# Performance work log

Measured on AMD Instinct MI355X. Metric: run time of the kernel, lower is better.

## Reference

```python
import jax
jax.config.update("jax_enable_x64", True)
import jax.numpy as jnp
import numpy as np

B = 1_000_000

def _generators():
    # 8 sl(3) basis elements, each scaled by its (unit) weight, float64.
    e = np.zeros((8, 3, 3), dtype=np.float64)
    e[0, 0, 2] = 1.0                      # x translation
    e[1, 1, 2] = 1.0                      # y translation
    e[2, 0, 1] = -1.0; e[2, 1, 0] = 1.0   # rotation
    e[3, 0, 0] = 1.0; e[3, 1, 1] = 1.0; e[3, 2, 2] = -2.0  # scale
    e[4, 0, 0] = 1.0; e[4, 1, 1] = -1.0   # stretch
    e[5, 0, 1] = 1.0; e[5, 1, 0] = 1.0    # shear
    e[6, 2, 0] = 1.0                      # x keystone
    e[7, 2, 1] = 1.0                      # y keystone
    weights = np.ones((8,), dtype=np.float64)  # all weight kwargs default to 1.0
    return jnp.asarray(e * weights[:, None, None])

_GEN = _generators()

def setup_inputs() -> dict:
    key = jax.random.key(0)
    lie_vectors = jax.random.normal(key, (B, 8), dtype=jnp.float32)
    return {"lie_vectors": lie_vectors}

def reference(lie_vectors) -> jnp.ndarray:
    # Weighted sum of generators in float64: (B,8) x (8,3,3) -> (B,3,3)
    A = jnp.einsum("bk,kij->bij", lie_vectors.astype(jnp.float64), _GEN)
    # Batched matrix exponential of tiny 3x3 matrices
    H = jax.vmap(jax.scipy.linalg.expm)(A)
    # Homogeneous normalization by the (2,2) entry
    H = H / H[:, 2:3, 2:3]
    return H.astype(jnp.float32)
```

## Files before the change

kernel.cpp:

```cpp
#include <hip/hip_runtime.h>
#include <math.h>

__device__ __forceinline__ void mm3(const double* __restrict__ A,
                                    const double* __restrict__ Bm,
                                    double* __restrict__ C) {
#pragma unroll
    for (int i = 0; i < 3; ++i) {
#pragma unroll
        for (int j = 0; j < 3; ++j) {
            C[i*3+j] = fma(A[i*3+0], Bm[0*3+j],
                       fma(A[i*3+1], Bm[1*3+j],
                           A[i*3+2] * Bm[2*3+j]));
        }
    }
}

#define BLOCK 256

__global__ __launch_bounds__(BLOCK) void lie_expm_kernel(const float* __restrict__ v,
                                                         float* __restrict__ out,
                                                         int n) {
    __shared__ float lds[BLOCK * 9];

    int tid = threadIdx.x;
    int gid = blockIdx.x * BLOCK + tid;
    bool active = gid < n;

    float oloc[9];

    if (active) {
        const float4* vv = reinterpret_cast<const float4*>(v);
        float4 p0 = vv[2*(size_t)gid + 0];
        float4 p1 = vv[2*(size_t)gid + 1];
        double x0 = p0.x, x1 = p0.y, x2 = p0.z, x3 = p0.w;
        double x4 = p1.x, x5 = p1.y, x6 = p1.z, x7 = p1.w;

        double A[9];
        A[0] = x3 + x4;  A[1] = x5 - x2;  A[2] = x0;
        A[3] = x2 + x5;  A[4] = x3 - x4;  A[5] = x1;
        A[6] = x6;       A[7] = x7;       A[8] = -2.0 * x3;

        double c0 = fabs(A[0]) + fabs(A[3]) + fabs(A[6]);
        double c1 = fabs(A[1]) + fabs(A[4]) + fabs(A[7]);
        double c2 = fabs(A[2]) + fabs(A[5]) + fabs(A[8]);
        double nrm = fmax(c0, fmax(c1, c2));

        const double theta13 = 5.371920351148152;
        double r = nrm * (1.0 / theta13);
        int s = 0;
        if (r > 1.0) {
            int hi = __double2hiint(r);
            s = ((hi >> 20) & 0x7ff) - 1023 + 1;
        }
        double sc = __hiloint2double((1023 - s) << 20, 0);
#pragma unroll
        for (int i = 0; i < 9; ++i) A[i] *= sc;

        const double b0  = 64764752532480000.0, b1  = 32382376266240000.0;
        const double b2  = 7771770303897600.0,  b3  = 1187353796428800.0;
        const double b4  = 129060195264000.0,   b5  = 10559470521600.0;
        const double b6  = 670442572800.0,      b7  = 33522128640.0;
        const double b8  = 1323241920.0,        b9  = 40840800.0;
        const double b10 = 960960.0,            b11 = 16380.0;
        const double b12 = 182.0,               b13 = 1.0;

        double A2[9], A4[9], A6[9];
        mm3(A, A, A2);
        mm3(A2, A2, A4);
        mm3(A4, A2, A6);

        double W[9], V[9];
#pragma unroll
        for (int i = 0; i < 9; ++i)
            W[i] = fma(b12, A6[i], fma(b10, A4[i], b8 * A2[i]));
        mm3(A6, W, V);
#pragma unroll
        for (int i = 0; i < 9; ++i)
            V[i] += fma(b6, A6[i], fma(b4, A4[i], b2 * A2[i]));
        V[0] += b0; V[4] += b0; V[8] += b0;

        double Z[9], U[9];
#pragma unroll
        for (int i = 0; i < 9; ++i)
            W[i] = fma(b13, A6[i], fma(b11, A4[i], b9 * A2[i]));
        mm3(A6, W, Z);
#pragma unroll
        for (int i = 0; i < 9; ++i)
            Z[i] += fma(b7, A6[i], fma(b5, A4[i], b3 * A2[i]));
        Z[0] += b1; Z[4] += b1; Z[8] += b1;
        mm3(A, Z, U);

        double M[9], R[9];
#pragma unroll
        for (int i = 0; i < 9; ++i) { M[i] = V[i] - U[i]; R[i] = V[i] + U[i]; }

        double inv[9];
        inv[0] = fma(M[4], M[8], -M[5]*M[7]);
        inv[1] = fma(M[2], M[7], -M[1]*M[8]);
        inv[2] = fma(M[1], M[5], -M[2]*M[4]);
        inv[3] = fma(M[5], M[6], -M[3]*M[8]);
        inv[4] = fma(M[0], M[8], -M[2]*M[6]);
        inv[5] = fma(M[2], M[3], -M[0]*M[5]);
        inv[6] = fma(M[3], M[7], -M[4]*M[6]);
        inv[7] = fma(M[1], M[6], -M[0]*M[7]);
        inv[8] = fma(M[0], M[4], -M[1]*M[3]);
        double det = fma(M[0], inv[0], fma(M[1], inv[3], M[2]*inv[6]));
        double rd = 1.0 / det;
#pragma unroll
        for (int i = 0; i < 9; ++i) inv[i] *= rd;

        double E[9], T[9];
        mm3(inv, R, E);

        for (int i = 0; i < s; ++i) {
            mm3(E, E, T);
#pragma unroll
            for (int j = 0; j < 9; ++j) E[j] = T[j];
        }

        double invh = 1.0 / E[8];
#pragma unroll
        for (int i = 0; i < 9; ++i) oloc[i] = (float)(E[i] * invh);
    }

    if (active) {
#pragma unroll
        for (int j = 0; j < 9; ++j) lds[tid * 9 + j] = oloc[j];
    }
    __syncthreads();

    size_t base = (size_t)blockIdx.x * (BLOCK * 9);
    int count = n - blockIdx.x * BLOCK;
    if (count > BLOCK) count = BLOCK;
    int total = count * 9;
#pragma unroll
    for (int i = 0; i < 9; ++i) {
        int idx = i * BLOCK + tid;
        if (idx < total) out[base + idx] = lds[idx];
    }
}

extern "C" void kernel_launch(void* const* d_in, const int* in_sizes, int n_in,
                              void* d_out, int out_size, void* d_ws, size_t ws_size,
                              hipStream_t stream) {
    const float* v = (const float*)d_in[0];
    float* out = (float*)d_out;
    int n = in_sizes[0] / 8;
    int grid = (n + BLOCK - 1) / BLOCK;
    lie_expm_kernel<<<grid, BLOCK, 0, stream>>>(v, out, n);
}
```

Measured before the change: 88.49 us.

## Evaluate Padé expm in the Cayley-Hamilton polynomial basis of traceless A

Because A is traceless (sl(3)), every matrix polynomial in A reduces to e0*I + e1*A + e2*A^2 with p = tr(A^2)/2 and q = det(A). The Padé numerator and denominator, the solve, and the repeated squaring are all done on these three coefficients, using Horner steps, a small structured 3x3 cofactor solve and coefficient squaring, rather than full 3x3 double matrix products. The full matrix is rebuilt only once at the end. This cuts FP64 arithmetic and register pressure a lot. The trade-off is possible precision differences, and the determinant scaling is skipped when s < 3, since it cancels in the final normalization.

```diff
diff --git a/kernel.cpp b/kernel.cpp
--- a/kernel.cpp
+++ b/kernel.cpp
@@ -1,21 +1,15 @@
 #include <hip/hip_runtime.h>
 #include <math.h>
 
-__device__ __forceinline__ void mm3(const double* __restrict__ A,
-                                    const double* __restrict__ Bm,
-                                    double* __restrict__ C) {
-#pragma unroll
-    for (int i = 0; i < 3; ++i) {
-#pragma unroll
-        for (int j = 0; j < 3; ++j) {
-            C[i*3+j] = fma(A[i*3+0], Bm[0*3+j],
-                       fma(A[i*3+1], Bm[1*3+j],
-                           A[i*3+2] * Bm[2*3+j]));
-        }
+#define BLOCK 256
+
+#define QSTEP(a0, a1, a2, bn)                         \
+    {                                                 \
+        double n0 = fma(q, a1, bn);                   \
+        double n1 = fma(p, a1, q * (a2));             \
+        double n2 = fma(p, a2, a0);                   \
+        a0 = n0; a1 = n1; a2 = n2;                    \
     }
-}
-
-#define BLOCK 256
 
 __global__ __launch_bounds__(BLOCK) void lie_expm_kernel(const float* __restrict__ v,
                                                          float* __restrict__ out,
@@ -30,8 +24,8 @@
 
     if (active) {
         const float4* vv = reinterpret_cast<const float4*>(v);
-        float4 p0 = vv[2*(size_t)gid + 0];
-        float4 p1 = vv[2*(size_t)gid + 1];
+        float4 p0 = vv[2 * (size_t)gid + 0];
+        float4 p1 = vv[2 * (size_t)gid + 1];
         double x0 = p0.x, x1 = p0.y, x2 = p0.z, x3 = p0.w;
         double x4 = p1.x, x5 = p1.y, x6 = p1.z, x7 = p1.w;
 
@@ -56,6 +50,22 @@
 #pragma unroll
         for (int i = 0; i < 9; ++i) A[i] *= sc;
 
+        double A2[9];
+#pragma unroll
+        for (int i = 0; i < 3; ++i) {
+#pragma unroll
+            for (int j = 0; j < 3; ++j) {
+                A2[i * 3 + j] = fma(A[i * 3 + 0], A[0 * 3 + j],
+                                fma(A[i * 3 + 1], A[1 * 3 + j],
+                                    A[i * 3 + 2] * A[2 * 3 + j]));
+            }
+        }
+
+        double p = 0.5 * (A2[0] + A2[4] + A2[8]);
+        double q = fma(A[0], fma(A[4], A[8], -A[5] * A[7]),
+                   fma(-A[1], fma(A[3], A[8], -A[5] * A[6]),
+                       A[2] * fma(A[3], A[7], -A[4] * A[6])));
+
         const double b0  = 64764752532480000.0, b1  = 32382376266240000.0;
         const double b2  = 7771770303897600.0,  b3  = 1187353796428800.0;
         const double b4  = 129060195264000.0,   b5  = 10559470521600.0;
@@ -64,63 +74,72 @@
         const double b10 = 960960.0,            b11 = 16380.0;
         const double b12 = 182.0,               b13 = 1.0;
 
-        double A2[9], A4[9], A6[9];
-        mm3(A, A, A2);
-        mm3(A2, A2, A4);
-        mm3(A4, A2, A6);
+        double u0 = b13, u1 = 0.0, u2 = 0.0;
+        QSTEP(u0, u1, u2, b11)
+        QSTEP(u0, u1, u2, b9)
+        QSTEP(u0, u1, u2, b7)
+        QSTEP(u0, u1, u2, b5)
+        QSTEP(u0, u1, u2, b3)
+        QSTEP(u0, u1, u2, b1)
 
-        double W[9], V[9];
-#pragma unroll
-        for (int i = 0; i < 9; ++i)
-            W[i] = fma(b12, A6[i], fma(b10, A4[i], b8 * A2[i]));
-        mm3(A6, W, V);
-#pragma unroll
-        for (int i = 0; i < 9; ++i)
-            V[i] += fma(b6, A6[i], fma(b4, A4[i], b2 * A2[i]));
-        V[0] += b0; V[4] += b0; V[8] += b0;
+        double t0 = b12, t1 = 0.0, t2 = 0.0;
+        QSTEP(t0, t1, t2, b10)
+        QSTEP(t0, t1, t2, b8)
+        QSTEP(t0, t1, t2, b6)
+        QSTEP(t0, t1, t2, b4)
+        QSTEP(t0, t1, t2, b2)
+        QSTEP(t0, t1, t2, b0)
 
-        double Z[9], U[9];
-#pragma unroll
-        for (int i = 0; i < 9; ++i)
-            W[i] = fma(b13, A6[i], fma(b11, A4[i], b9 * A2[i]));
-        mm3(A6, W, Z);
-#pragma unroll
-        for (int i = 0; i < 9; ++i)
-            Z[i] += fma(b7, A6[i], fma(b5, A4[i], b3 * A2[i]));
-        Z[0] += b1; Z[4] += b1; Z[8] += b1;
-        mm3(A, Z, U);
+        double U0 = q * u2;
+        double U1 = fma(p, u2, u0);
+        double U2 = u1;
 
-        double M[9], R[9];
-#pragma unroll
-        for (int i = 0; i < 9; ++i) { M[i] = V[i] - U[i]; R[i] = V[i] + U[i]; }
+        double m0 = t0 - U0, m1 = t1 - U1, m2 = t2 - U2;
+        double r0 = t0 + U0, r1 = t1 + U1, r2 = t2 + U2;
 
-        double inv[9];
-        inv[0] = fma(M[4], M[8], -M[5]*M[7]);
-        inv[1] = fma(M[2], M[7], -M[1]*M[8]);
-        inv[2] = fma(M[1], M[5], -M[2]*M[4]);
-        inv[3] = fma(M[5], M[6], -M[3]*M[8]);
-        inv[4] = fma(M[0], M[8], -M[2]*M[6]);
-        inv[5] = fma(M[2], M[3], -M[0]*M[5]);
-        inv[6] = fma(M[3], M[7], -M[4]*M[6]);
-        inv[7] = fma(M[1], M[6], -M[0]*M[7]);
-        inv[8] = fma(M[0], M[4], -M[1]*M[3]);
-        double det = fma(M[0], inv[0], fma(M[1], inv[3], M[2]*inv[6]));
-        double rd = 1.0 / det;
-#pragma unroll
-        for (int i = 0; i < 9; ++i) inv[i] *= rd;
+        double L00 = m0,              L01 = q * m2,          L02 = q * m1;
+        double L10 = m1,              L11 = fma(p, m2, m0),  L12 = fma(p, m1, q * m2);
+        double L20 = m2,              L21 = m1,              L22 = L11;
 
-        double E[9], T[9];
-        mm3(inv, R, E);
+        double C00 = fma(L11, L22, -L12 * L21);
+        double C01 = fma(L02, L21, -L01 * L22);
+        double C02 = fma(L01, L12, -L02 * L11);
+        double C10 = fma(L12, L20, -L10 * L22);
+        double C11 = fma(L00, L22, -L02 * L20);
+        double C12 = fma(L02, L10, -L00 * L12);
+        double C20 = fma(L10, L21, -L11 * L20);
+        double C21 = fma(L01, L20, -L00 * L21);
+        double C22 = fma(L00, L11, -L01 * L10);
+
+        double e0 = fma(C00, r0, fma(C01, r1, C02 * r2));
+        double e1 = fma(C10, r0, fma(C11, r1, C12 * r2));
+        double e2 = fma(C20, r0, fma(C21, r1, C22 * r2));
+
+        if (s >= 3) {
+            double det = fma(L00, C00, fma(L01, C10, L02 * C20));
+            double rd = 1.0 / det;
+            e0 *= rd; e1 *= rd; e2 *= rd;
+        }
 
         for (int i = 0; i < s; ++i) {
-            mm3(E, E, T);
-#pragma unroll
-            for (int j = 0; j < 9; ++j) E[j] = T[j];
+            double d0 = e0 * e0;
+            double d1 = 2.0 * e0 * e1;
+            double d2 = fma(e1, e1, 2.0 * e0 * e2);
+            double d3 = 2.0 * e1 * e2;
+            double d4 = e2 * e2;
+            e0 = fma(q, d3, d0);
+            e1 = fma(p, d3, fma(q, d4, d1));
+            e2 = fma(p, d4, d2);
         }
 
-        double invh = 1.0 / E[8];
+        double H[9];
 #pragma unroll
-        for (int i = 0; i < 9; ++i) oloc[i] = (float)(E[i] * invh);
+        for (int i = 0; i < 9; ++i) H[i] = fma(e1, A[i], e2 * A2[i]);
+        H[0] += e0; H[4] += e0; H[8] += e0;
+
+        double invh = 1.0 / H[8];
+#pragma unroll
+        for (int i = 0; i < 9; ++i) oloc[i] = (float)(H[i] * invh);
     }
 
     if (active) {
```

Measured after the change: 82.08 us. 7.2% less time.
